# Kernel tuning notes

Hardware: AMD Instinct MI355X
Metric: run time of the kernel (lower is better)

## Reference

```python
import jax, jax.numpy as jnp
import numpy as np

H, W = 224, 224
NF, IN_NF, NL = 32, 100, 4


def conv2d(x, w):
    # 3x3 same-padding conv, NCHW / OIHW
    return jax.lax.conv_general_dilated(x, w, (1, 1), [(1, 1), (1, 1)],
                                        dimension_numbers=('NCHW', 'OIHW', 'NCHW'))


def prelu(x, a):
    return jnp.where(x >= 0, x, a[None, :, None, None] * x)


def bilinear_warp(x, flow):
    # backward warp: sample x at (grid + flow), border clamping
    B, C, Hh, Ww = x.shape
    yy, xx = jnp.meshgrid(jnp.arange(Hh, dtype=x.dtype), jnp.arange(Ww, dtype=x.dtype), indexing='ij')
    px = xx[None] + flow[:, 0]  # [B,H,W]
    py = yy[None] + flow[:, 1]
    x0 = jnp.floor(px); y0 = jnp.floor(py)
    wx = (px - x0)[:, None]; wy = (py - y0)[:, None]  # [B,1,H,W]
    cx = lambda v: jnp.clip(v, 0, Ww - 1).astype(jnp.int32)
    cy = lambda v: jnp.clip(v, 0, Hh - 1).astype(jnp.int32)
    x0i, x1i = cx(x0), cx(x0 + 1)
    y0i, y1i = cy(y0), cy(y0 + 1)
    gather = jax.vmap(lambda img, yi, xi: img[:, yi, xi])  # per-batch fancy gather -> [C,H,W]
    I00 = gather(x, y0i, x0i); I01 = gather(x, y0i, x1i)
    I10 = gather(x, y1i, x0i); I11 = gather(x, y1i, x1i)
    return I00 * (1 - wx) * (1 - wy) + I01 * wx * (1 - wy) + I10 * (1 - wx) * wy + I11 * wx * wy


def glblock_forward(feat_0, feat_1, feat_dense, flow, space_mask,
                    w_head, a_head, w_blocks, a_blocks, w_last, b_last, w_mask, b_mask):
    f0w = bilinear_warp(feat_0, flow[:, :2])
    f1w = bilinear_warp(feat_1, flow[:, 2:4])
    x = jnp.concatenate([f0w, f1w, feat_dense, flow], axis=1)  # [1, in_nf, H, W]
    mask_up = jnp.repeat(jnp.repeat(space_mask, 2, axis=2), 2, axis=3)
    # head: conv3x3 (no bias) + PReLU, then spatial masking
    x = prelu(conv2d(x, w_head), a_head) * space_mask
    outs = [x]
    for i in range(w_blocks.shape[0]):
        x = prelu(conv2d(x, w_blocks[i]) * space_mask, a_blocks[i])
        outs.append(x)
    feats = jnp.concatenate(outs, axis=1)  # [1, in_nf*(NL+1), H, W]
    x = jnp.einsum('oi,bihw->bohw', w_last, feats) + b_last[None, :, None, None]  # 1x1 conv
    smn = conv2d(x[:, 4:], w_mask) + b_mask[None, :, None, None]  # [1,2,H,W]
    B, C, Hh, Ww = x.shape
    xu = jax.image.resize(x, (B, C, 2 * Hh, 2 * Ww), 'linear')
    smnu = jax.image.resize(smn, (B, 2, 2 * Hh, 2 * Ww), 'linear')
    flow_out = xu[:, :4]
    feat_t = xu[:, 4:]
    # eval-mode hard routing mask (training uses gumbel-softmax)
    mask_next = (smnu[:, :1] > smnu[:, 1:]).astype(x.dtype) * mask_up
    return flow_out, feat_t, mask_next


def setup_inputs() -> dict:
    key = jax.random.key(0)
    ks = jax.random.split(key, 12)
    r = lambda i, shape, s=1.0: jax.random.normal(ks[i], shape, jnp.float32) * s
    return {
        'feat_0': r(0, (1, NF, H, W)),
        'feat_1': r(1, (1, NF, H, W)),
        'feat_dense': r(2, (1, NF, H, W)),
        'flow': r(3, (1, 4, H, W)),
        'space_mask': jax.random.uniform(ks[4], (1, 1, H, W), jnp.float32),
        'w_head': r(5, (IN_NF, IN_NF, 3, 3), 0.02),
        'a_head': jnp.full((IN_NF,), 0.25, jnp.float32),
        'w_blocks': r(6, (NL, IN_NF, IN_NF, 3, 3), 0.02),
        'a_blocks': jnp.full((NL, IN_NF), 0.25, jnp.float32),
        'w_last': r(7, (4 + NF, IN_NF * (NL + 1)), 0.02),
        'b_last': r(8, (4 + NF,), 0.02),
        'w_mask': r(9, (2, NF, 3, 3), 0.02),
        'b_mask': r(10, (2,), 0.02),
    }


def reference(feat_0, feat_1, feat_dense, flow, space_mask,
              w_head, a_head, w_blocks, a_blocks, w_last, b_last, w_mask, b_mask):
    return glblock_forward(feat_0, feat_1, feat_dense, flow, space_mask,
                           w_head, a_head, w_blocks, a_blocks, w_last, b_last, w_mask, b_mask)
```

## Files before the change

### kernel.cpp

```cpp
#include <hip/hip_runtime.h>
#include <hip/hip_bf16.h>

#define HWs 50176
#define WID 224
#define OHW 200704

typedef __attribute__((ext_vector_type(8))) short s16x8;
typedef __attribute__((ext_vector_type(4))) float f32x4;

static __device__ __forceinline__ unsigned short f2bf(float x) {
  unsigned u = __float_as_uint(x);
  unsigned r = (u + 0x7fffu + ((u >> 16) & 1u)) >> 16;
  return (unsigned short)r;
}
static __device__ __forceinline__ float bf2f(unsigned short b) {
  return __uint_as_float(((unsigned)b) << 16);
}

__global__ void k_wt(const float* __restrict__ w_head, const float* __restrict__ w_blk,
                     unsigned short* __restrict__ bw) {
  int gid = blockIdx.x * 256 + threadIdx.x;
  int frag = gid >> 7, rr = gid & 127;
  int spl = rr >> 6, lane = rr & 63;
  int l = frag / 288, q = frag - l * 288;
  int t = q / 32, q2 = q - t * 32;
  int ck = q2 >> 3, nt = q2 & 7;
  int oc = nt * 16 + (lane & 15);
  int kg = lane >> 4;
  const float* src = (l == 0) ? w_head : (w_blk + (size_t)(l - 1) * 90000);
  s16x8 outv;
  #pragma unroll
  for (int e = 0; e < 8; ++e) {
    int ic = ck * 32 + kg * 8 + e;
    float w = (oc < 100 && ic < 100) ? src[oc * 900 + ic * 9 + t] : 0.f;
    unsigned short h = f2bf(w);
    unsigned short lo = f2bf(w - bf2f(h));
    outv[e] = (short)(spl ? lo : h);
  }
  ((s16x8*)bw)[gid] = outv;
}

__global__ void k_wlT(const float* __restrict__ wlast, float* __restrict__ wlT) {
  int i = blockIdx.x * 256 + threadIdx.x;
  if (i < 18000) {
    int il = i / 36, o = i - il * 36;
    wlT[i] = wlast[o * 500 + il];
  }
}

__global__ void k_warp(const float* __restrict__ f0, const float* __restrict__ f1,
                       const float* __restrict__ fd, const float* __restrict__ fl,
                       float* __restrict__ xin) {
  int p = blockIdx.x * 256 + threadIdx.x;
  int yq = blockIdx.y;
  int y = p / WID, x = p - y * WID;
  float fx0 = fl[p];
  float fy0 = fl[HWs + p];
  float fx1 = fl[2 * HWs + p];
  float fy1 = fl[3 * HWs + p];

  #pragma unroll
  for (int img = 0; img < 2; ++img) {
    const float* src = img ? f1 : f0;
    float fx = img ? fx1 : fx0;
    float fy = img ? fy1 : fy0;
    float px = (float)x + fx, py = (float)y + fy;
    float x0f = floorf(px), y0f = floorf(py);
    float wx = px - x0f, wy = py - y0f;
    int x0 = (int)fminf(fmaxf(x0f,       0.f), 223.f);
    int x1 = (int)fminf(fmaxf(x0f + 1.f, 0.f), 223.f);
    int y0 = (int)fminf(fmaxf(y0f,       0.f), 223.f);
    int y1 = (int)fminf(fmaxf(y0f + 1.f, 0.f), 223.f);
    float w00 = (1.f - wx) * (1.f - wy), w01 = wx * (1.f - wy);
    float w10 = (1.f - wx) * wy,         w11 = wx * wy;
    int i00 = y0 * WID + x0, i01 = y0 * WID + x1;
    int i10 = y1 * WID + x0, i11 = y1 * WID + x1;
    float* dst = xin + img * 32 * HWs;
    for (int c = yq * 8; c < yq * 8 + 8; ++c) {
      const float* pl = src + c * HWs;
      dst[c * HWs + p] = w00 * pl[i00] + w01 * pl[i01]
                       + w10 * pl[i10] + w11 * pl[i11];
    }
  }
  for (int c = yq * 8; c < yq * 8 + 8; ++c)
    xin[(64 + c) * HWs + p] = fd[c * HWs + p];
  if (yq == 0) {
    xin[96 * HWs + p] = fx0; xin[97 * HWs + p] = fy0;
    xin[98 * HWs + p] = fx1; xin[99 * HWs + p] = fy1;
  }
}

__global__ __launch_bounds__(256) void k_conv(
    const float* __restrict__ in, const unsigned short* __restrict__ bw,
    const float* __restrict__ avec, const float* __restrict__ mask,
    float* __restrict__ out) {
  __shared__ __align__(16) unsigned char sh[2][6 * 34 * 160];
  const int tid = threadIdx.x;
  const int lane = tid & 63;
  const int wv = tid >> 6;
  const int wr = wv >> 1, wz = wv & 1;
  const int c0 = blockIdx.x * 32;
  const int r0 = blockIdx.y * 4;
  const int li = lane & 15, kg = lane >> 4;

  f32x4 acc[4][4];
  #pragma unroll
  for (int a = 0; a < 4; ++a)
    #pragma unroll
    for (int b = 0; b < 4; ++b) acc[a][b] = (f32x4){0.f, 0.f, 0.f, 0.f};

  const s16x8* bp = (const s16x8*)bw;
  s16x8 bcur[4][2], bnxt[4][2];
  #pragma unroll
  for (int nt = 0; nt < 4; ++nt)
    #pragma unroll
    for (int sp = 0; sp < 2; ++sp)
      bnxt[nt][sp] = bp[(((wz * 4 + nt) * 2 + sp) << 6) + lane];

  auto STAGE = [&](int ck, unsigned char* dst) {
    for (int j = tid; j < 816; j += 256) {
      int kgs = j & 3;
      int rc = j >> 2;
      int pr = rc / 34, pc = rc - pr * 34;
      int gy = r0 - 1 + pr, gx = c0 - 1 + pc;
      int gb = ck * 32 + kgs * 8;
      bool inb = ((unsigned)gy < 224u) && ((unsigned)gx < 224u);
      const float* src = in + (size_t)gb * HWs + gy * WID + gx;
      s16x8 hv, lv;
      #pragma unroll
      for (int e = 0; e < 8; ++e) {
        float v = 0.f;
        if (inb && (gb + e) < 100) v = src[(size_t)e * HWs];
        unsigned short h = f2bf(v);
        unsigned short l2 = f2bf(v - bf2f(h));
        hv[e] = (short)h; lv[e] = (short)l2;
      }
      int base = rc * 160, sw = (rc & 7) << 4;
      *(s16x8*)(dst + base + ((kgs * 16) ^ sw)) = hv;
      *(s16x8*)(dst + base + ((64 + kgs * 16) ^ sw)) = lv;
    }
  };

  STAGE(0, sh[0]);
  __syncthreads();

  for (int ck = 0; ck < 4; ++ck) {
    unsigned char* cur = sh[ck & 1];
    if (ck < 3) STAGE(ck + 1, sh[(ck + 1) & 1]);

    #pragma unroll
    for (int t = 0; t < 9; ++t) {
      #pragma unroll
      for (int nt = 0; nt < 4; ++nt) {
        bcur[nt][0] = bnxt[nt][0];
        bcur[nt][1] = bnxt[nt][1];
      }
      if (t < 8 || ck < 3) {
        int nf = (t < 8) ? (t + 1) * 32 + ck * 8 : (ck + 1) * 8;
        #pragma unroll
        for (int nt = 0; nt < 4; ++nt)
          #pragma unroll
          for (int sp = 0; sp < 2; ++sp)
            bnxt[nt][sp] = bp[(((nf + wz * 4 + nt) * 2 + sp) << 6) + lane];
      }
      const int dy = t / 3 - 1, dx = t - (t / 3) * 3 - 1;
      #pragma unroll
      for (int ms = 0; ms < 4; ++ms) {
        int pr = wr * 2 + (ms >> 1) + 1 + dy;
        int pc = (ms & 1) * 16 + li + 1 + dx;
        int rc = pr * 34 + pc;
        int base = rc * 160, sw = (rc & 7) << 4;
        s16x8 ah = *(const s16x8*)(cur + base + ((kg * 16) ^ sw));
        s16x8 al = *(const s16x8*)(cur + base + ((64 + kg * 16) ^ sw));
        #pragma unroll
        for (int nt = 0; nt < 4; ++nt) {
          acc[ms][nt] = __builtin_amdgcn_mfma_f32_16x16x32_bf16(ah, bcur[nt][0], acc[ms][nt], 0, 0, 0);
          acc[ms][nt] = __builtin_amdgcn_mfma_f32_16x16x32_bf16(al, bcur[nt][0], acc[ms][nt], 0, 0, 0);
          acc[ms][nt] = __builtin_amdgcn_mfma_f32_16x16x32_bf16(ah, bcur[nt][1], acc[ms][nt], 0, 0, 0);
        }
      }
    }
    __syncthreads();
  }

  float4 mv[4];
  #pragma unroll
  for (int ms = 0; ms < 4; ++ms) {
    int row = r0 + wr * 2 + (ms >> 1);
    int colb = c0 + (ms & 1) * 16 + kg * 4;
    mv[ms] = *(const float4*)&mask[row * WID + colb];
  }
  #pragma unroll
  for (int nt = 0; nt < 4; ++nt) {
    int oc = wz * 64 + nt * 16 + li;
    if (oc < 100) {
      float a = avec[oc];
      #pragma unroll
      for (int ms = 0; ms < 4; ++ms) {
        int row = r0 + wr * 2 + (ms >> 1);
        int colb = c0 + (ms & 1) * 16 + kg * 4;
        f32x4 zv = acc[ms][nt];
        float4 o;
        o.x = (zv.x >= 0.f ? zv.x : a * zv.x) * mv[ms].x;
        o.y = (zv.y >= 0.f ? zv.y : a * zv.y) * mv[ms].y;
        o.z = (zv.z >= 0.f ? zv.z : a * zv.z) * mv[ms].z;
        o.w = (zv.w >= 0.f ? zv.w : a * zv.w) * mv[ms].w;
        *(float4*)&out[(size_t)oc * HWs + row * WID + colb] = o;
      }
    }
  }
}

__global__ __launch_bounds__(256) void k_einsum(
    const float* __restrict__ A0, const float* __restrict__ A1,
    const float* __restrict__ A2, const float* __restrict__ A3,
    const float* __restrict__ A4, const float* __restrict__ wlT,
    const float* __restrict__ blast, float* __restrict__ xlast) {
  int p = blockIdx.x * 256 + threadIdx.x;
  float acc[36];
  #pragma unroll
  for (int o = 0; o < 36; ++o) acc[o] = blast[o];
  const float* bufs[5] = {A0, A1, A2, A3, A4};
  #pragma unroll
  for (int l = 0; l < 5; ++l) {
    const float* a = bufs[l] + p;
    const float* w = wlT + l * 3600;
    for (int oc4 = 0; oc4 < 100; oc4 += 4) {
      float v0 = a[(size_t)(oc4 + 0) * HWs];
      float v1 = a[(size_t)(oc4 + 1) * HWs];
      float v2 = a[(size_t)(oc4 + 2) * HWs];
      float v3 = a[(size_t)(oc4 + 3) * HWs];
      #pragma unroll
      for (int q = 0; q < 4; ++q) {
        float v = (q == 0) ? v0 : (q == 1) ? v1 : (q == 2) ? v2 : v3;
        const float4* wp = (const float4*)(w + (oc4 + q) * 36);
        #pragma unroll
        for (int j = 0; j < 9; ++j) {
          float4 t = wp[j];
          acc[4*j]   = fmaf(t.x, v, acc[4*j]);
          acc[4*j+1] = fmaf(t.y, v, acc[4*j+1]);
          acc[4*j+2] = fmaf(t.z, v, acc[4*j+2]);
          acc[4*j+3] = fmaf(t.w, v, acc[4*j+3]);
        }
      }
    }
  }
  #pragma unroll
  for (int o = 0; o < 36; ++o) xlast[(size_t)o * HWs + p] = acc[o];
}

__global__ void k_smn(const float* __restrict__ xlast, const float* __restrict__ wmask,
                      const float* __restrict__ bmask, float* __restrict__ smnh) {
  __shared__ float wm[288];
  int tid = threadIdx.x;
  int h = blockIdx.y;
  for (int j = tid; j < 288; j += 64) {
    int o = j / 144, r = j - o * 144;
    wm[j] = wmask[o * 288 + h * 144 + r];
  }
  __syncthreads();
  int p = blockIdx.x * 64 + tid;
  int y = p / WID, x = p - y * WID;
  double a0 = 0.0, a1 = 0.0;
  for (int icl = 0; icl < 16; ++icl) {
    const float* pl = xlast + (size_t)(4 + h * 16 + icl) * HWs;
    #pragma unroll
    for (int dy = -1; dy <= 1; ++dy) {
      int gy = y + dy;
      if ((unsigned)gy < 224u) {
        #pragma unroll
        for (int dx = -1; dx <= 1; ++dx) {
          int gx = x + dx;
          if ((unsigned)gx < 224u) {
            double v = (double)pl[gy * WID + gx];
            int t = (dy + 1) * 3 + (dx + 1);
            a0 += (double)wm[icl * 9 + t] * v;
            a1 += (double)wm[144 + icl * 9 + t] * v;
          }
        }
      }
    }
  }
  if (h == 0) { a0 += (double)bmask[0]; a1 += (double)bmask[1]; }
  smnh[(size_t)(h * 2 + 0) * HWs + p] = (float)a0;
  smnh[(size_t)(h * 2 + 1) * HWs + p] = (float)a1;
}

__global__ void k_upsample(const float* __restrict__ xlast, const float* __restrict__ smnh,
                           const float* __restrict__ smask, float* __restrict__ out) {
  int q = blockIdx.x * 256 + threadIdx.x;
  int oy = q / 448, ox = q - oy * 448;
  int ky = oy >> 1, kx = ox >> 1;
  int r0, r1, c0, c1; float wy0, wy1, wx0, wx1;
  if (oy & 1) { r0 = ky; r1 = (ky < 223) ? ky + 1 : 223; wy0 = 0.75f; wy1 = 0.25f; }
  else        { r0 = (ky > 0) ? ky - 1 : 0; r1 = ky;     wy0 = 0.25f; wy1 = 0.75f; }
  if (ox & 1) { c0 = kx; c1 = (kx < 223) ? kx + 1 : 223; wx0 = 0.75f; wx1 = 0.25f; }
  else        { c0 = (kx > 0) ? kx - 1 : 0; c1 = kx;     wx0 = 0.25f; wx1 = 0.75f; }
  float w00 = wy0 * wx0, w01 = wy0 * wx1, w10 = wy1 * wx0, w11 = wy1 * wx1;
  int i00 = r0 * WID + c0, i01 = r0 * WID + c1, i10 = r1 * WID + c0, i11 = r1 * WID + c1;
  for (int ch = 0; ch < 36; ++ch) {
    const float* pl = xlast + (size_t)ch * HWs;
    out[(size_t)ch * OHW + q] = w00 * pl[i00] + w01 * pl[i01]
                              + w10 * pl[i10] + w11 * pl[i11];
  }
  const float* sa0 = smnh;
  const float* sa1 = smnh + HWs;
  const float* sb0 = smnh + 2 * HWs;
  const float* sb1 = smnh + 3 * HWs;
  double s0 = (double)w00 * ((double)sa0[i00] + (double)sb0[i00])
            + (double)w01 * ((double)sa0[i01] + (double)sb0[i01])
            + (double)w10 * ((double)sa0[i10] + (double)sb0[i10])
            + (double)w11 * ((double)sa0[i11] + (double)sb0[i11]);
  double s1 = (double)w00 * ((double)sa1[i00] + (double)sb1[i00])
            + (double)w01 * ((double)sa1[i01] + (double)sb1[i01])
            + (double)w10 * ((double)sa1[i10] + (double)sb1[i10])
            + (double)w11 * ((double)sa1[i11] + (double)sb1[i11]);
  float mu = smask[ky * WID + kx];
  out[36 * OHW + q] = (s0 > s1) ? mu : 0.f;
}

extern "C" void kernel_launch(void* const* d_in, const int* in_sizes, int n_in,
                              void* d_out, int out_size, void* d_ws, size_t ws_size,
                              hipStream_t stream) {
  const float* feat0   = (const float*)d_in[0];
  const float* feat1   = (const float*)d_in[1];
  const float* featd   = (const float*)d_in[2];
  const float* flow    = (const float*)d_in[3];
  const float* smask   = (const float*)d_in[4];
  const float* w_head  = (const float*)d_in[5];
  const float* a_head  = (const float*)d_in[6];
  const float* w_blk   = (const float*)d_in[7];
  const float* a_blk   = (const float*)d_in[8];
  const float* w_last  = (const float*)d_in[9];
  const float* b_last  = (const float*)d_in[10];
  const float* w_mask  = (const float*)d_in[11];
  const float* b_mask  = (const float*)d_in[12];

  float* B0 = (float*)d_ws;
  float* B1 = B0 + (size_t)100 * HWs;
  float* B2 = B1 + (size_t)100 * HWs;
  float* B3 = B2 + (size_t)100 * HWs;
  float* B4 = B3 + (size_t)100 * HWs;
  float* smnh = B4 + (size_t)100 * HWs;
  float* wlT  = smnh + (size_t)4 * HWs;
  float* xlast = wlT + 18000;
  unsigned short* bw = (unsigned short*)xlast;

  k_wt<<<dim3(720), 256, 0, stream>>>(w_head, w_blk, bw);
  k_wlT<<<dim3(71), 256, 0, stream>>>(w_last, wlT);
  k_warp<<<dim3(196, 4), 256, 0, stream>>>(feat0, feat1, featd, flow, B0);

  dim3 cgrid(7, 56);
  k_conv<<<cgrid, 256, 0, stream>>>(B0, bw,               a_head,      smask, B1);
  k_conv<<<cgrid, 256, 0, stream>>>(B1, bw + 1 * 294912,  a_blk,       smask, B0);
  k_conv<<<cgrid, 256, 0, stream>>>(B0, bw + 2 * 294912,  a_blk + 100, smask, B2);
  k_conv<<<cgrid, 256, 0, stream>>>(B2, bw + 3 * 294912,  a_blk + 200, smask, B3);
  k_conv<<<cgrid, 256, 0, stream>>>(B3, bw + 4 * 294912,  a_blk + 300, smask, B4);

  k_einsum<<<dim3(196), 256, 0, stream>>>(B1, B0, B2, B3, B4, wlT, b_last, xlast);

  k_smn<<<dim3(784, 2), 64, 0, stream>>>(xlast, w_mask, b_mask, smnh);
  k_upsample<<<784, 256, 0, stream>>>(xlast, smnh, smask, (float*)d_out);
}
```

Baseline: 510.1 us.

## Split 1x1 einsum across layers with atomic accumulation and bias-init kernel

The 1x1 einsum over the 500 concatenated channels previously ran as 196 blocks of 256 threads, with each thread looping over all five feature buffers. The work is now split by input buffer across a second grid dimension, using 784x5 blocks of 64 threads. Partial sums are combined with fp32 atomicAdd into an output that a separate kernel pre-fills with the bias. This aims to fix under-occupancy of the GPU during a bandwidth-heavy reduction, in exchange for an extra launch, atomic traffic, and summation order that is no longer deterministic.

```diff
diff --git a/kernel.cpp b/kernel.cpp
--- a/kernel.cpp
+++ b/kernel.cpp
@@ -46,6 +46,11 @@
     int il = i / 36, o = i - il * 36;
     wlT[i] = wlast[o * 500 + il];
   }
+}
+
+__global__ void k_binit(const float* __restrict__ blast, float* __restrict__ xlast) {
+  int p = blockIdx.x * 256 + threadIdx.x;
+  xlast[(size_t)blockIdx.y * HWs + p] = blast[blockIdx.y];
 }
 
 __global__ void k_warp(const float* __restrict__ f0, const float* __restrict__ f1,
@@ -211,42 +216,39 @@
   }
 }
 
-__global__ __launch_bounds__(256) void k_einsum(
+__global__ __launch_bounds__(64) void k_esum(
     const float* __restrict__ A0, const float* __restrict__ A1,
     const float* __restrict__ A2, const float* __restrict__ A3,
     const float* __restrict__ A4, const float* __restrict__ wlT,
-    const float* __restrict__ blast, float* __restrict__ xlast) {
-  int p = blockIdx.x * 256 + threadIdx.x;
+    float* __restrict__ xlast) {
+  int p = blockIdx.x * 64 + threadIdx.x;
+  int l = blockIdx.y;
+  const float* a = (l == 0) ? A0 : (l == 1) ? A1 : (l == 2) ? A2 : (l == 3) ? A3 : A4;
+  const float* w = wlT + l * 3600;
   float acc[36];
   #pragma unroll
-  for (int o = 0; o < 36; ++o) acc[o] = blast[o];
-  const float* bufs[5] = {A0, A1, A2, A3, A4};
-  #pragma unroll
-  for (int l = 0; l < 5; ++l) {
-    const float* a = bufs[l] + p;
-    const float* w = wlT + l * 3600;
-    for (int oc4 = 0; oc4 < 100; oc4 += 4) {
-      float v0 = a[(size_t)(oc4 + 0) * HWs];
-      float v1 = a[(size_t)(oc4 + 1) * HWs];
-      float v2 = a[(size_t)(oc4 + 2) * HWs];
-      float v3 = a[(size_t)(oc4 + 3) * HWs];
-      #pragma unroll
-      for (int q = 0; q < 4; ++q) {
-        float v = (q == 0) ? v0 : (q == 1) ? v1 : (q == 2) ? v2 : v3;
-        const float4* wp = (const float4*)(w + (oc4 + q) * 36);
-        #pragma unroll
-        for (int j = 0; j < 9; ++j) {
-          float4 t = wp[j];
-          acc[4*j]   = fmaf(t.x, v, acc[4*j]);
-          acc[4*j+1] = fmaf(t.y, v, acc[4*j+1]);
-          acc[4*j+2] = fmaf(t.z, v, acc[4*j+2]);
-          acc[4*j+3] = fmaf(t.w, v, acc[4*j+3]);
-        }
-      }
-    }
-  }
-  #pragma unroll
-  for (int o = 0; o < 36; ++o) xlast[(size_t)o * HWs + p] = acc[o];
+  for (int o = 0; o < 36; ++o) acc[o] = 0.f;
+  for (int c0 = 0; c0 < 100; c0 += 10) {
+    float v[10];
+    #pragma unroll
+    for (int q = 0; q < 10; ++q)
+      v[q] = a[(size_t)(c0 + q) * HWs + p];
+    #pragma unroll
+    for (int q = 0; q < 10; ++q) {
+      const float4* wp = (const float4*)(w + (c0 + q) * 36);
+      #pragma unroll
+      for (int j = 0; j < 9; ++j) {
+        float4 t = wp[j];
+        acc[4*j]   = fmaf(t.x, v[q], acc[4*j]);
+        acc[4*j+1] = fmaf(t.y, v[q], acc[4*j+1]);
+        acc[4*j+2] = fmaf(t.z, v[q], acc[4*j+2]);
+        acc[4*j+3] = fmaf(t.w, v[q], acc[4*j+3]);
+      }
+    }
+  }
+  #pragma unroll
+  for (int o = 0; o < 36; ++o)
+    atomicAdd(&xlast[(size_t)o * HWs + p], acc[o]);
 }
 
 __global__ void k_smn(const float* __restrict__ xlast, const float* __restrict__ wmask,
@@ -357,7 +359,8 @@
   k_conv<<<cgrid, 256, 0, stream>>>(B2, bw + 3 * 294912,  a_blk + 200, smask, B3);
   k_conv<<<cgrid, 256, 0, stream>>>(B3, bw + 4 * 294912,  a_blk + 300, smask, B4);
 
-  k_einsum<<<dim3(196), 256, 0, stream>>>(B1, B0, B2, B3, B4, wlT, b_last, xlast);
+  k_binit<<<dim3(196, 36), 256, 0, stream>>>(b_last, xlast);
+  k_esum<<<dim3(784, 5), 64, 0, stream>>>(B1, B0, B2, B3, B4, wlT, xlast);
 
   k_smn<<<dim3(784, 2), 64, 0, stream>>>(xlast, w_mask, b_mask, smnh);
   k_upsample<<<784, 256, 0, stream>>>(xlast, smnh, smask, (float*)d_out);
```

New measurement: 462.7 us. 9.3% less time.
